# Performance work log

Hardware: AMD Instinct MI355X
Metric: run time of the kernel (lower is better)

Reference implementation:

```python
import jax, jax.numpy as jnp
import numpy as np


def _lin(key, fin, fout):
    return jax.random.normal(key, (fin, fout), jnp.float32) / np.sqrt(fin)


def _hgt_conv(x, Wk, bk, Wq, bq, Wv, bv, a_rel, m_rel, p_rel, Wo, bo, skip, src, dst):
    # Faithful single-(node,edge)-type PyG HGTConv.
    N = x.shape[0]
    H, D = a_rel.shape[0], a_rel.shape[1]
    k = (x @ Wk + bk).reshape(N, H, D)
    q = (x @ Wq + bq).reshape(N, H, D)
    v = (x @ Wv + bv).reshape(N, H, D)
    # per-edge-type relation transforms (per-head DxD matrices)
    k = jnp.einsum('nhd,hde->nhe', k, a_rel)
    v = jnp.einsum('nhd,hde->nhe', v, m_rel)
    # attention logits per edge (j=src -> i=dst), [E,H]
    alpha = (q[dst] * k[src]).sum(-1) * p_rel / jnp.sqrt(jnp.asarray(D, x.dtype))
    # segment softmax over incoming edges of each dst node
    amax = jax.ops.segment_max(alpha, dst, num_segments=N)
    amax = jnp.where(jnp.isfinite(amax), amax, 0.0)  # empty segments
    ex = jnp.exp(alpha - amax[dst])
    denom = jax.ops.segment_sum(ex, dst, num_segments=N)
    w = ex / denom[dst]                                   # [E,H]
    agg = jax.ops.segment_sum(v[src] * w[..., None], dst, num_segments=N)
    out = jax.nn.gelu(agg.reshape(N, H * D), approximate=False) @ Wo + bo
    a = jax.nn.sigmoid(skip)  # trainable skip (in == out channels)
    return a * out + (1.0 - a) * x


def _decode(z, ei, Wlp, blp):
    src, dst = ei[0], ei[1]
    feat = jnp.concatenate([z[src], z[dst]], axis=1)
    return (feat @ Wlp + blp).squeeze(-1)


def setup_inputs() -> dict:
    N, E, P = 50000, 800000, 100000
    C, H = 128, 4
    D = C // H
    ks = jax.random.split(jax.random.key(0), 32)
    inp = {}
    inp['x'] = jax.random.normal(ks[0], (N, C), jnp.float32)
    inp['edge_index'] = jax.random.randint(ks[1], (2, E), 0, N, jnp.int32)
    inp['edge_weight'] = jax.random.uniform(ks[2], (E,), jnp.float32)
    inp['pos_edge_index'] = jax.random.randint(ks[3], (2, P), 0, N, jnp.int32)
    inp['neg_edge_index'] = jax.random.randint(ks[4], (2, P), 0, N, jnp.int32)
    i = 5
    for l in (1, 2):
        for nm in ('k', 'q', 'v'):
            inp[f'W{l}{nm}'] = _lin(ks[i], C, C); i += 1
            inp[f'b{l}{nm}'] = jnp.zeros((C,), jnp.float32)
        inp[f'a{l}'] = jax.random.normal(ks[i], (H, D, D), jnp.float32) / np.sqrt(D); i += 1
        inp[f'm{l}'] = jax.random.normal(ks[i], (H, D, D), jnp.float32) / np.sqrt(D); i += 1
        inp[f'p{l}'] = jnp.ones((H,), jnp.float32)
        inp[f'Wo{l}'] = _lin(ks[i], C, C); i += 1
        inp[f'bo{l}'] = jnp.zeros((C,), jnp.float32)
        inp[f'skip{l}'] = jnp.ones((), jnp.float32)
    inp['Wlp'] = _lin(ks[i], 2 * C, 1)
    inp['blp'] = jnp.zeros((1,), jnp.float32)
    return inp


def reference(x, edge_index, edge_weight, pos_edge_index, neg_edge_index,
              W1k, b1k, W1q, b1q, W1v, b1v, a1, m1, p1, Wo1, bo1, skip1,
              W2k, b2k, W2q, b2q, W2v, b2v, a2, m2, p2, Wo2, bo2, skip2,
              Wlp, blp):
    src, dst = edge_index[0], edge_index[1]
    h1 = _hgt_conv(x, W1k, b1k, W1q, b1q, W1v, b1v, a1, m1, p1, Wo1, bo1, skip1, src, dst)
    h2 = _hgt_conv(h1, W2k, b2k, W2q, b2q, W2v, b2v, a2, m2, p2, Wo2, bo2, skip2, src, dst)
    pos = _decode(h2, pos_edge_index, Wlp, blp)
    neg = _decode(h2, neg_edge_index, Wlp, blp)
    return (pos, neg)
```

## Files before the change

### kernel.cpp

```cpp
#include <hip/hip_runtime.h>
#include <hip/hip_bf16.h>

#define CDIV(a,b) (((a)+(b)-1)/(b))

typedef __attribute__((ext_vector_type(8))) short bh8;
typedef __attribute__((ext_vector_type(4))) float f32x4;

__device__ __forceinline__ float gelu_exact(float x){
  return 0.5f * x * (1.0f + erff(x * 0.7071067811865475f));
}
__device__ __forceinline__ float blo(unsigned u){ return __uint_as_float(u << 16); }
__device__ __forceinline__ float bhi(unsigned u){ return __uint_as_float(u & 0xFFFF0000u); }
__device__ __forceinline__ unsigned short bf16bits(float x){
  __hip_bfloat16 b = __float2bfloat16(x);
  return *(unsigned short*)&b;
}

__global__ void k_clear_int(int* __restrict__ p, int n){
  int i = blockIdx.x*256 + threadIdx.x;
  if (i < n) p[i] = 0;
}

__global__ void k_deg(const int* __restrict__ dst, int* __restrict__ deg, int E){
  int e = blockIdx.x*256 + threadIdx.x;
  if (e < E) atomicAdd(&deg[dst[e]], 1);
}

__global__ void k_scan_blk(const int* __restrict__ deg, int* __restrict__ rowp,
                           int* __restrict__ partial, int N){
  __shared__ int buf[256];
  int i = blockIdx.x*256 + threadIdx.x;
  int v = (i < N) ? deg[i] : 0;
  buf[threadIdx.x] = v;
  __syncthreads();
  #pragma unroll
  for (int off = 1; off < 256; off <<= 1){
    int t = (threadIdx.x >= off) ? buf[threadIdx.x - off] : 0;
    __syncthreads();
    buf[threadIdx.x] += t;
    __syncthreads();
  }
  if (i < N) rowp[i] = buf[threadIdx.x] - v;
  if (threadIdx.x == 255) partial[blockIdx.x] = buf[255];
}

__global__ void k_scan_fin(int* __restrict__ rowp, const int* __restrict__ partial,
                           int* __restrict__ cursor, int N, int E, int nb){
  __shared__ int ws[4];
  int t = threadIdx.x;
  int v = (t < nb && t < blockIdx.x) ? partial[t] : 0;
  #pragma unroll
  for (int m = 32; m; m >>= 1) v += __shfl_xor(v, m);
  if ((t & 63) == 0) ws[t >> 6] = v;
  __syncthreads();
  int pre = ws[0] + ws[1] + ws[2] + ws[3];
  int i = blockIdx.x*256 + t;
  if (i < N){
    int nv = rowp[i] + pre;
    rowp[i] = nv;
    cursor[i] = nv;
  }
  if (i == 0) rowp[N] = E;
}

__global__ void k_fill(const int* __restrict__ src, const int* __restrict__ dst,
                       int* __restrict__ cursor, int* __restrict__ srcs, int E){
  int e = blockIdx.x*256 + threadIdx.x;
  if (e >= E) return;
  int d = dst[e];
  int pos = atomicAdd(&cursor[d], 1);
  srcs[pos] = src[e];
}

__global__ void k_prep(const float* __restrict__ Wk, const float* __restrict__ bk,
                       const float* __restrict__ Ak, const float* __restrict__ Wq,
                       const float* __restrict__ Wv, const float* __restrict__ bv,
                       const float* __restrict__ Av, const float* __restrict__ Wo,
                       short* __restrict__ BfH,
                       float* __restrict__ beffK, float* __restrict__ beffV){
  int t = blockIdx.x*256 + threadIdx.x;
  if (t < 4*16384){
    int g = t >> 14;
    int u = t & 16383;
    int k = u & 127, n = u >> 7;
    float x;
    if (g == 1)      x = Wq[(size_t)k*128 + n];
    else if (g == 3) x = Wo[(size_t)k*128 + n];
    else {
      const float* W = (g == 0) ? Wk : Wv;
      const float* A = (g == 0) ? Ak : Av;
      int h = n >> 5, e2 = n & 31;
      const float* s  = W + (size_t)k*128 + h*32;
      const float* Ah = A + h*1024 + e2;
      float acc = 0.f;
      #pragma unroll
      for (int d = 0; d < 32; ++d) acc += s[d] * Ah[d*32];
      x = acc;
    }
    int nt = n >> 4, lr = n & 15, ks = k >> 5, lk = (k >> 3) & 3, e = k & 7;
    size_t o = ((size_t)((g*8 + nt)*4 + ks)*64 + lr*4 + lk)*8 + e;
    BfH[o] = (short)bf16bits(x);
  } else {
    int u = t - 4*16384;
    if (u < 256){
      int which = u >> 7, n = u & 127;
      const float* b = which ? bv : bk;
      const float* A = which ? Av : Ak;
      int h = n >> 5, e2 = n & 31;
      const float* Ah = A + h*1024 + e2;
      float acc = 0.f;
      #pragma unroll
      for (int d = 0; d < 32; ++d) acc += b[h*32 + d] * Ah[d*32];
      (which ? beffV : beffK)[n] = acc;
    }
  }
}

__global__ __launch_bounds__(256)
void k_kqv(const float* __restrict__ A,
           const short* __restrict__ BfH,
           const float* __restrict__ bK, const float* __restrict__ bQ,
           const float* __restrict__ bV,
           unsigned short* __restrict__ KV16, unsigned short* __restrict__ Qb16, int M){
  const int tid = threadIdx.x;
  const int wm = tid >> 6, l = tid & 63;
  const int lr = l & 15, lk = l >> 4;
  const int perm = (lr*4 + lk)*8;
  const int p0 = blockIdx.x*8 + wm*2;

  bh8 a_h[2][4], a_l[2][4];
  #pragma unroll
  for (int p = 0; p < 2; ++p){
    int row = (p0 + p)*16 + lr;
    #pragma unroll
    for (int ks = 0; ks < 4; ++ks){
      float f[8] = {0.f,0.f,0.f,0.f,0.f,0.f,0.f,0.f};
      if (row < M){
        float4 va = *(const float4*)(A + (size_t)row*128 + ks*32 + lk*8);
        float4 vb = *(const float4*)(A + (size_t)row*128 + ks*32 + lk*8 + 4);
        f[0]=va.x; f[1]=va.y; f[2]=va.z; f[3]=va.w;
        f[4]=vb.x; f[5]=vb.y; f[6]=vb.z; f[7]=vb.w;
      }
      bh8 h8, l8;
      #pragma unroll
      for (int q = 0; q < 8; ++q){
        unsigned ub = __float_as_uint(f[q]);
        h8[q] = (short)(ub >> 16);
        float fhv = __uint_as_float(ub & 0xFFFF0000u);
        l8[q] = (short)(__float_as_uint(f[q] - fhv) >> 16);
      }
      a_h[p][ks] = h8;
      a_l[p][ks] = l8;
    }
  }

  #pragma unroll
  for (int g = 0; g < 3; ++g){
    f32x4 acc[2][8];
    #pragma unroll
    for (int p = 0; p < 2; ++p)
      #pragma unroll
      for (int i = 0; i < 8; ++i) acc[p][i] = (f32x4){0.f,0.f,0.f,0.f};
    #pragma unroll
    for (int ks = 0; ks < 4; ++ks){
      #pragma unroll
      for (int nt = 0; nt < 8; ++nt){
        size_t o = (size_t)((g*8 + nt)*4 + ks)*512 + perm;
        bh8 bh_ = *(const bh8*)(BfH + o);
        #pragma unroll
        for (int p = 0; p < 2; ++p){
          acc[p][nt] = __builtin_amdgcn_mfma_f32_16x16x32_bf16(bh_, a_h[p][ks], acc[p][nt], 0, 0, 0);
          acc[p][nt] = __builtin_amdgcn_mfma_f32_16x16x32_bf16(bh_, a_l[p][ks], acc[p][nt], 0, 0, 0);
        }
      }
    }
    const float* bias = (g==0) ? bK : (g==1) ? bQ : bV;
    #pragma unroll
    for (int p = 0; p < 2; ++p){
      int r = (p0 + p)*16 + lr;
      if (r >= M) continue;
      #pragma unroll
      for (int nt = 0; nt < 8; ++nt){
        int c0 = nt*16 + lk*4;
        float4 bs = *(const float4*)(bias + c0);
        float v0 = acc[p][nt][0] + bs.x;
        float v1 = acc[p][nt][1] + bs.y;
        float v2 = acc[p][nt][2] + bs.z;
        float v3 = acc[p][nt][3] + bs.w;
        unsigned u0 = (unsigned)bf16bits(v0) | ((unsigned)bf16bits(v1) << 16);
        unsigned u1 = (unsigned)bf16bits(v2) | ((unsigned)bf16bits(v3) << 16);
        if (g == 1){
          *(uint2*)(Qb16 + (size_t)r*128 + c0) = make_uint2(u0, u1);
        } else {
          *(uint2*)(KV16 + (size_t)r*256 + (size_t)(nt*4 + lk)*8 + ((g == 2) ? 4 : 0))
              = make_uint2(u0, u1);
        }
      }
    }
  }
}

template<bool DECODE>
__global__ __launch_bounds__(256)
void k_outgemm(const short* __restrict__ AfH,
               const short* __restrict__ BfH,
               const float* __restrict__ bias, const float* __restrict__ mixsrc,
               const float* __restrict__ skipp, float* __restrict__ out,
               const float* __restrict__ Wlp,
               float* __restrict__ s1, float* __restrict__ s2, int M){
  const int tid = threadIdx.x;
  const int wm = tid >> 6, l = tid & 63;
  const int lr = l & 15, lk = l >> 4;
  const int perm = (lr*4 + lk)*8;
  const int p0 = blockIdx.x*8 + wm*2;

  bh8 a_h[2][4];
  #pragma unroll
  for (int p = 0; p < 2; ++p)
    #pragma unroll
    for (int ks = 0; ks < 4; ++ks){
      size_t o = (size_t)((p0 + p)*4 + ks)*512 + perm;
      a_h[p][ks] = *(const bh8*)(AfH + o);
    }

  f32x4 acc[2][8];
  #pragma unroll
  for (int p = 0; p < 2; ++p)
    #pragma unroll
    for (int i = 0; i < 8; ++i) acc[p][i] = (f32x4){0.f,0.f,0.f,0.f};
  #pragma unroll
  for (int ks = 0; ks < 4; ++ks){
    #pragma unroll
    for (int nt = 0; nt < 8; ++nt){
      size_t o = (size_t)((3*8 + nt)*4 + ks)*512 + perm;
      bh8 bh_ = *(const bh8*)(BfH + o);
      #pragma unroll
      for (int p = 0; p < 2; ++p){
        acc[p][nt] = __builtin_amdgcn_mfma_f32_16x16x32_bf16(bh_, a_h[p][ks], acc[p][nt], 0, 0, 0);
      }
    }
  }
  float sg = 1.f / (1.f + expf(-skipp[0]));
  #pragma unroll
  for (int p = 0; p < 2; ++p){
    int r = (p0 + p)*16 + lr;
    if (r >= M) continue;
    float d1 = 0.f, d2 = 0.f;
    #pragma unroll
    for (int nt = 0; nt < 8; ++nt){
      int c0 = nt*16 + lk*4;
      float4 bs  = *(const float4*)(bias + c0);
      float4 mx  = *(const float4*)(mixsrc + (size_t)r*128 + c0);
      float4 o4;
      o4.x = sg*(acc[p][nt][0] + bs.x) + (1.f - sg)*mx.x;
      o4.y = sg*(acc[p][nt][1] + bs.y) + (1.f - sg)*mx.y;
      o4.z = sg*(acc[p][nt][2] + bs.z) + (1.f - sg)*mx.z;
      o4.w = sg*(acc[p][nt][3] + bs.w) + (1.f - sg)*mx.w;
      if (DECODE){
        float4 w1 = *(const float4*)(Wlp + c0);
        float4 w2 = *(const float4*)(Wlp + 128 + c0);
        d1 += o4.x*w1.x + o4.y*w1.y + o4.z*w1.z + o4.w*w1.w;
        d2 += o4.x*w2.x + o4.y*w2.y + o4.z*w2.z + o4.w*w2.w;
      } else {
        *(float4*)(out + (size_t)r*128 + c0) = o4;
      }
    }
    if (DECODE){
      d1 += __shfl_xor(d1, 16); d1 += __shfl_xor(d1, 32);
      d2 += __shfl_xor(d2, 16); d2 += __shfl_xor(d2, 32);
      if (lk == 0){ s1[r] = d1; s2[r] = d2; }
    }
  }
}

__global__ __launch_bounds__(256)
void k_node(const unsigned short* __restrict__ KV, const unsigned short* __restrict__ Qb,
            const int* __restrict__ srcs, const int* __restrict__ row_ptr,
            const float* __restrict__ p,
            short* __restrict__ fh, int NN){
  int wave = threadIdx.x >> 6;
  int lane = threadIdx.x & 63;
  int L = lane & 31;
  int node = blockIdx.x*8 + wave*2 + (lane >> 5);
  if (node >= NN) return;
  int start = row_ptr[node], end = row_ptr[node+1];
  int h = L >> 3;
  float ph = p[h] * 0.25504366769049834f;
  const unsigned short* KVl = KV + L*8;
  uint2 qu = *(const uint2*)(Qb + (size_t)node*128 + L*4);
  float4 qv = make_float4(blo(qu.x), bhi(qu.x), blo(qu.y), bhi(qu.y));

  float a0=0.f, a1=0.f, a2=0.f, a3=0.f, den=0.f;
  int j = start;
  for (; j + 3 < end; j += 4){
    int s0 = srcs[j], s1 = srcs[j+1], s2 = srcs[j+2], s3 = srcs[j+3];
    uint4 kv0 = *(const uint4*)(KVl + (size_t)s0*256);
    uint4 kv1 = *(const uint4*)(KVl + (size_t)s1*256);
    uint4 kv2 = *(const uint4*)(KVl + (size_t)s2*256);
    uint4 kv3 = *(const uint4*)(KVl + (size_t)s3*256);
    float d0 = blo(kv0.x)*qv.x + bhi(kv0.x)*qv.y + blo(kv0.y)*qv.z + bhi(kv0.y)*qv.w;
    float d1 = blo(kv1.x)*qv.x + bhi(kv1.x)*qv.y + blo(kv1.y)*qv.z + bhi(kv1.y)*qv.w;
    float d2 = blo(kv2.x)*qv.x + bhi(kv2.x)*qv.y + blo(kv2.y)*qv.z + bhi(kv2.y)*qv.w;
    float d3 = blo(kv3.x)*qv.x + bhi(kv3.x)*qv.y + blo(kv3.y)*qv.z + bhi(kv3.y)*qv.w;
    #pragma unroll
    for (int m = 1; m < 8; m <<= 1){
      d0 += __shfl_xor(d0, m);
      d1 += __shfl_xor(d1, m);
      d2 += __shfl_xor(d2, m);
      d3 += __shfl_xor(d3, m);
    }
    float w0 = exp2f(d0 * ph);
    float w1 = exp2f(d1 * ph);
    float w2 = exp2f(d2 * ph);
    float w3 = exp2f(d3 * ph);
    den += (w0 + w1) + (w2 + w3);
    a0 += (w0*blo(kv0.z) + w1*blo(kv1.z)) + (w2*blo(kv2.z) + w3*blo(kv3.z));
    a1 += (w0*bhi(kv0.z) + w1*bhi(kv1.z)) + (w2*bhi(kv2.z) + w3*bhi(kv3.z));
    a2 += (w0*blo(kv0.w) + w1*blo(kv1.w)) + (w2*blo(kv2.w) + w3*blo(kv3.w));
    a3 += (w0*bhi(kv0.w) + w1*bhi(kv1.w)) + (w2*bhi(kv2.w) + w3*bhi(kv3.w));
  }
  for (; j < end; ++j){
    int s0 = srcs[j];
    uint4 kv0 = *(const uint4*)(KVl + (size_t)s0*256);
    float d0 = blo(kv0.x)*qv.x + bhi(kv0.x)*qv.y + blo(kv0.y)*qv.z + bhi(kv0.y)*qv.w;
    #pragma unroll
    for (int m = 1; m < 8; m <<= 1) d0 += __shfl_xor(d0, m);
    float w0 = exp2f(d0 * ph);
    den += w0;
    a0 += w0*blo(kv0.z);
    a1 += w0*bhi(kv0.z);
    a2 += w0*blo(kv0.w);
    a3 += w0*bhi(kv0.w);
  }
  float o[4] = {0.f, 0.f, 0.f, 0.f};
  if (end > start){
    float inv = 1.f / den;
    o[0] = gelu_exact(a0 * inv);
    o[1] = gelu_exact(a1 * inv);
    o[2] = gelu_exact(a2 * inv);
    o[3] = gelu_exact(a3 * inv);
  }
  size_t ci = (size_t)((node >> 4)*4 + h)*64 + (node & 15)*4 + ((L >> 1) & 3);
  size_t si = ci*8 + (L & 1)*4;
  uint2 uh = make_uint2((unsigned)bf16bits(o[0]) | ((unsigned)bf16bits(o[1]) << 16),
                        (unsigned)bf16bits(o[2]) | ((unsigned)bf16bits(o[3]) << 16));
  *(uint2*)(fh + si) = uh;
}

__global__ void k_decode(const int* __restrict__ pe, const int* __restrict__ ne,
                         const float* __restrict__ s1, const float* __restrict__ s2,
                         const float* __restrict__ blp, float* __restrict__ out, int P){
  int i = blockIdx.x*256 + threadIdx.x;
  if (i < P){
    out[i] = s1[pe[i]] + s2[pe[P + i]] + blp[0];
  } else if (i < 2*P){
    int j = i - P;
    out[P + j] = s1[ne[j]] + s2[ne[P + j]] + blp[0];
  }
}

extern "C" void kernel_launch(void* const* d_in, const int* in_sizes, int n_in,
                              void* d_out, int out_size, void* d_ws, size_t ws_size,
                              hipStream_t stream){
  const float* x      = (const float*)d_in[0];
  const int*   ei     = (const int*)d_in[1];
  const int*   pos_ei = (const int*)d_in[3];
  const int*   neg_ei = (const int*)d_in[4];
  const int NN = in_sizes[0] / 128;
  const int E  = in_sizes[1] / 2;
  const int P  = in_sizes[3] / 2;
  const int padM = CDIV(NN, 128) * 128;
  const int* e_src = ei;
  const int* e_dst = ei + E;

  char* wsb = (char*)d_ws;
  size_t off = 0;
  auto alloc = [&](size_t bytes)->char*{
    char* r = wsb + off;
    off = (off + bytes + 255) & ~(size_t)255;
    return r;
  };
  unsigned short* KV16 = (unsigned short*)alloc((size_t)NN*256*2);
  unsigned short* Qb16 = (unsigned short*)alloc((size_t)NN*128*2);
  float* h1     = (float*)alloc((size_t)NN*128*4);
  short* AfH    = (short*)alloc((size_t)padM*128*2);
  int*   srcs   = (int*)alloc((size_t)E*4);
  int*   rowp   = (int*)alloc((size_t)(NN+1)*4);
  int*   deg    = (int*)alloc((size_t)NN*4);
  int*   cursor = (int*)alloc((size_t)NN*4);
  int*   partial= (int*)alloc(256*4);
  float* beffK1 = (float*)alloc(128*4);
  float* beffV1 = (float*)alloc(128*4);
  float* beffK2 = (float*)alloc(128*4);
  float* beffV2 = (float*)alloc(128*4);
  short* BfH1   = (short*)alloc((size_t)4*16384*2);
  short* BfH2   = (short*)alloc((size_t)4*16384*2);
  float* s1     = (float*)alloc((size_t)NN*4);
  float* s2     = (float*)alloc((size_t)NN*4);

  const int nb = CDIV(NN, 256);
  k_clear_int<<<CDIV(NN,256),256,0,stream>>>(deg, NN);
  k_deg<<<CDIV(E,256),256,0,stream>>>(e_dst, deg, E);
  k_scan_blk<<<nb,256,0,stream>>>(deg, rowp, partial, NN);
  k_scan_fin<<<nb,256,0,stream>>>(rowp, partial, cursor, NN, E, nb);
  k_fill<<<CDIV(E,256),256,0,stream>>>(e_src, e_dst, cursor, srcs, E);
  k_prep<<<CDIV(4*16384+256,256),256,0,stream>>>(
      (const float*)d_in[5],  (const float*)d_in[6],  (const float*)d_in[11],
      (const float*)d_in[7],  (const float*)d_in[9],  (const float*)d_in[10],
      (const float*)d_in[12], (const float*)d_in[14],
      BfH1, beffK1, beffV1);
  k_prep<<<CDIV(4*16384+256,256),256,0,stream>>>(
      (const float*)d_in[17], (const float*)d_in[18], (const float*)d_in[23],
      (const float*)d_in[19], (const float*)d_in[21], (const float*)d_in[22],
      (const float*)d_in[24], (const float*)d_in[26],
      BfH2, beffK2, beffV2);

  const int gblk = padM / 128;
  const float* Wlp = (const float*)d_in[29];

  k_kqv<<<gblk,256,0,stream>>>(x, BfH1, beffK1, (const float*)d_in[8], beffV1,
                               KV16, Qb16, NN);
  k_node<<<CDIV(NN,8),256,0,stream>>>(KV16, Qb16, srcs, rowp,
                                      (const float*)d_in[13], AfH, NN);
  k_outgemm<false><<<gblk,256,0,stream>>>(AfH, BfH1, (const float*)d_in[15], x,
                                          (const float*)d_in[16], h1,
                                          nullptr, nullptr, nullptr, NN);
  k_kqv<<<gblk,256,0,stream>>>(h1, BfH2, beffK2, (const float*)d_in[20], beffV2,
                               KV16, Qb16, NN);
  k_node<<<CDIV(NN,8),256,0,stream>>>(KV16, Qb16, srcs, rowp,
                                      (const float*)d_in[25], AfH, NN);
  k_outgemm<true><<<gblk,256,0,stream>>>(AfH, BfH2, (const float*)d_in[27], h1,
                                         (const float*)d_in[28], nullptr,
                                         Wlp, s1, s2, NN);

  k_decode<<<CDIV(2*P,256),256,0,stream>>>(pos_ei, neg_ei, s1, s2,
                                           (const float*)d_in[30], (float*)d_out, P);
}
```

Baseline: 306.9 us.

## Drop split-bf16 input GEMM, store intermediate h1 as bf16, merge prep kernels

Removes the hi/lo bf16 split of the GEMM input in k_kqv, halving the MFMA count, and rounds the input to bf16 once instead. Layer-1 output h1 is written and read as bf16 rather than fp32, halving its traffic in the outgemm store, the second kqv load and the skip-mix read. The two weight-prep launches are merged into one. The cost is lower precision in the K/Q/V projections and in the residual path, which may push results closer to the tolerance.

```diff
diff --git a/kernel.cpp b/kernel.cpp
--- a/kernel.cpp
+++ b/kernel.cpp
@@ -72,17 +72,14 @@
   srcs[pos] = src[e];
 }
 
-__global__ void k_prep(const float* __restrict__ Wk, const float* __restrict__ bk,
-                       const float* __restrict__ Ak, const float* __restrict__ Wq,
-                       const float* __restrict__ Wv, const float* __restrict__ bv,
-                       const float* __restrict__ Av, const float* __restrict__ Wo,
-                       short* __restrict__ BfH,
-                       float* __restrict__ beffK, float* __restrict__ beffV){
-  int t = blockIdx.x*256 + threadIdx.x;
-  if (t < 4*16384){
-    int g = t >> 14;
-    int u = t & 16383;
-    int k = u & 127, n = u >> 7;
+__device__ __forceinline__ void prep_one(int u,
+    const float* Wk, const float* bk, const float* Ak, const float* Wq,
+    const float* Wv, const float* bv, const float* Av, const float* Wo,
+    short* BfH, float* beffK, float* beffV){
+  if (u < 4*16384){
+    int g = u >> 14;
+    int w = u & 16383;
+    int k = w & 127, n = w >> 7;
     float x;
     if (g == 1)      x = Wq[(size_t)k*128 + n];
     else if (g == 3) x = Wo[(size_t)k*128 + n];
@@ -101,9 +98,9 @@
     size_t o = ((size_t)((g*8 + nt)*4 + ks)*64 + lr*4 + lk)*8 + e;
     BfH[o] = (short)bf16bits(x);
   } else {
-    int u = t - 4*16384;
-    if (u < 256){
-      int which = u >> 7, n = u & 127;
+    int w = u - 4*16384;
+    if (w < 256){
+      int which = w >> 7, n = w & 127;
       const float* b = which ? bv : bk;
       const float* A = which ? Av : Ak;
       int h = n >> 5, e2 = n & 31;
@@ -116,8 +113,25 @@
   }
 }
 
+__global__ void k_prep2(
+    const float* Wk1, const float* bk1, const float* Ak1, const float* Wq1,
+    const float* Wv1, const float* bv1, const float* Av1, const float* Wo1,
+    const float* Wk2, const float* bk2, const float* Ak2, const float* Wq2,
+    const float* Wv2, const float* bv2, const float* Av2, const float* Wo2,
+    short* __restrict__ BfH1, short* __restrict__ BfH2,
+    float* __restrict__ beffK1, float* __restrict__ beffV1,
+    float* __restrict__ beffK2, float* __restrict__ beffV2){
+  const int SZ = 4*16384 + 256;
+  int t = blockIdx.x*256 + threadIdx.x;
+  if (t < SZ)
+    prep_one(t, Wk1, bk1, Ak1, Wq1, Wv1, bv1, Av1, Wo1, BfH1, beffK1, beffV1);
+  else if (t < 2*SZ)
+    prep_one(t - SZ, Wk2, bk2, Ak2, Wq2, Wv2, bv2, Av2, Wo2, BfH2, beffK2, beffV2);
+}
+
+template<bool BF16IN>
 __global__ __launch_bounds__(256)
-void k_kqv(const float* __restrict__ A,
+void k_kqv(const void* __restrict__ Ain,
            const short* __restrict__ BfH,
            const float* __restrict__ bK, const float* __restrict__ bQ,
            const float* __restrict__ bV,
@@ -128,29 +142,31 @@
   const int perm = (lr*4 + lk)*8;
   const int p0 = blockIdx.x*8 + wm*2;
 
-  bh8 a_h[2][4], a_l[2][4];
+  bh8 a_h[2][4];
   #pragma unroll
   for (int p = 0; p < 2; ++p){
     int row = (p0 + p)*16 + lr;
     #pragma unroll
     for (int ks = 0; ks < 4; ++ks){
-      float f[8] = {0.f,0.f,0.f,0.f,0.f,0.f,0.f,0.f};
-      if (row < M){
-        float4 va = *(const float4*)(A + (size_t)row*128 + ks*32 + lk*8);
-        float4 vb = *(const float4*)(A + (size_t)row*128 + ks*32 + lk*8 + 4);
-        f[0]=va.x; f[1]=va.y; f[2]=va.z; f[3]=va.w;
-        f[4]=vb.x; f[5]=vb.y; f[6]=vb.z; f[7]=vb.w;
-      }
-      bh8 h8, l8;
-      #pragma unroll
-      for (int q = 0; q < 8; ++q){
-        unsigned ub = __float_as_uint(f[q]);
-        h8[q] = (short)(ub >> 16);
-        float fhv = __uint_as_float(ub & 0xFFFF0000u);
-        l8[q] = (short)(__float_as_uint(f[q] - fhv) >> 16);
-      }
-      a_h[p][ks] = h8;
-      a_l[p][ks] = l8;
+      if (BF16IN){
+        bh8 z = (bh8){0,0,0,0,0,0,0,0};
+        if (row < M)
+          z = *(const bh8*)((const short*)Ain + (size_t)row*128 + ks*32 + lk*8);
+        a_h[p][ks] = z;
+      } else {
+        const float* A = (const float*)Ain;
+        float f[8] = {0.f,0.f,0.f,0.f,0.f,0.f,0.f,0.f};
+        if (row < M){
+          float4 va = *(const float4*)(A + (size_t)row*128 + ks*32 + lk*8);
+          float4 vb = *(const float4*)(A + (size_t)row*128 + ks*32 + lk*8 + 4);
+          f[0]=va.x; f[1]=va.y; f[2]=va.z; f[3]=va.w;
+          f[4]=vb.x; f[5]=vb.y; f[6]=vb.z; f[7]=vb.w;
+        }
+        bh8 h8;
+        #pragma unroll
+        for (int q = 0; q < 8; ++q) h8[q] = (short)bf16bits(f[q]);
+        a_h[p][ks] = h8;
+      }
     }
   }
 
@@ -170,7 +186,6 @@
         #pragma unroll
         for (int p = 0; p < 2; ++p){
           acc[p][nt] = __builtin_amdgcn_mfma_f32_16x16x32_bf16(bh_, a_h[p][ks], acc[p][nt], 0, 0, 0);
-          acc[p][nt] = __builtin_amdgcn_mfma_f32_16x16x32_bf16(bh_, a_l[p][ks], acc[p][nt], 0, 0, 0);
         }
       }
     }
@@ -200,12 +215,12 @@
   }
 }
 
-template<bool DECODE>
+template<bool DECODE, bool MIXBF16>
 __global__ __launch_bounds__(256)
 void k_outgemm(const short* __restrict__ AfH,
                const short* __restrict__ BfH,
-               const float* __restrict__ bias, const float* __restrict__ mixsrc,
-               const float* __restrict__ skipp, float* __restrict__ out,
+               const float* __restrict__ bias, const void* __restrict__ mixsrc,
+               const float* __restrict__ skipp, unsigned short* __restrict__ outb,
                const float* __restrict__ Wlp,
                float* __restrict__ s1, float* __restrict__ s2, int M){
   const int tid = threadIdx.x;
@@ -249,8 +264,14 @@
     #pragma unroll
     for (int nt = 0; nt < 8; ++nt){
       int c0 = nt*16 + lk*4;
-      float4 bs  = *(const float4*)(bias + c0);
-      float4 mx  = *(const float4*)(mixsrc + (size_t)r*128 + c0);
+      float4 bs = *(const float4*)(bias + c0);
+      float4 mx;
+      if (MIXBF16){
+        uint2 mu = *(const uint2*)((const unsigned short*)mixsrc + (size_t)r*128 + c0);
+        mx = make_float4(blo(mu.x), bhi(mu.x), blo(mu.y), bhi(mu.y));
+      } else {
+        mx = *(const float4*)((const float*)mixsrc + (size_t)r*128 + c0);
+      }
       float4 o4;
       o4.x = sg*(acc[p][nt][0] + bs.x) + (1.f - sg)*mx.x;
       o4.y = sg*(acc[p][nt][1] + bs.y) + (1.f - sg)*mx.y;
@@ -262,7 +283,9 @@
         d1 += o4.x*w1.x + o4.y*w1.y + o4.z*w1.z + o4.w*w1.w;
         d2 += o4.x*w2.x + o4.y*w2.y + o4.z*w2.z + o4.w*w2.w;
       } else {
-        *(float4*)(out + (size_t)r*128 + c0) = o4;
+        unsigned u0 = (unsigned)bf16bits(o4.x) | ((unsigned)bf16bits(o4.y) << 16);
+        unsigned u1 = (unsigned)bf16bits(o4.z) | ((unsigned)bf16bits(o4.w) << 16);
+        *(uint2*)(outb + (size_t)r*128 + c0) = make_uint2(u0, u1);
       }
     }
     if (DECODE){
@@ -382,7 +405,7 @@
   };
   unsigned short* KV16 = (unsigned short*)alloc((size_t)NN*256*2);
   unsigned short* Qb16 = (unsigned short*)alloc((size_t)NN*128*2);
-  float* h1     = (float*)alloc((size_t)NN*128*4);
+  unsigned short* h1b  = (unsigned short*)alloc((size_t)NN*128*2);
   short* AfH    = (short*)alloc((size_t)padM*128*2);
   int*   srcs   = (int*)alloc((size_t)E*4);
   int*   rowp   = (int*)alloc((size_t)(NN+1)*4);
@@ -404,34 +427,32 @@
   k_scan_blk<<<nb,256,0,stream>>>(deg, rowp, partial, NN);
   k_scan_fin<<<nb,256,0,stream>>>(rowp, partial, cursor, NN, E, nb);
   k_fill<<<CDIV(E,256),256,0,stream>>>(e_src, e_dst, cursor, srcs, E);
-  k_prep<<<CDIV(4*16384+256,256),256,0,stream>>>(
+  k_prep2<<<CDIV(2*(4*16384+256),256),256,0,stream>>>(
       (const float*)d_in[5],  (const float*)d_in[6],  (const float*)d_in[11],
       (const float*)d_in[7],  (const float*)d_in[9],  (const float*)d_in[10],
       (const float*)d_in[12], (const float*)d_in[14],
-      BfH1, beffK1, beffV1);
-  k_prep<<<CDIV(4*16384+256,256),256,0,stream>>>(
       (const float*)d_in[17], (const float*)d_in[18], (const float*)d_in[23],
       (const float*)d_in[19], (const float*)d_in[21], (const float*)d_in[22],
       (const float*)d_in[24], (const float*)d_in[26],
-      BfH2, beffK2, beffV2);
+      BfH1, BfH2, beffK1, beffV1, beffK2, beffV2);
 
   const int gblk = padM / 128;
   const float* Wlp = (const float*)d_in[29];
 
-  k_kqv<<<gblk,256,0,stream>>>(x, BfH1, beffK1, (const float*)d_in[8], beffV1,
-                               KV16, Qb16, NN);
+  k_kqv<false><<<gblk,256,0,stream>>>(x, BfH1, beffK1, (const float*)d_in[8], beffV1,
+                                      KV16, Qb16, NN);
   k_node<<<CDIV(NN,8),256,0,stream>>>(KV16, Qb16, srcs, rowp,
                                       (const float*)d_in[13], AfH, NN);
-  k_outgemm<false><<<gblk,256,0,stream>>>(AfH, BfH1, (const float*)d_in[15], x,
-                                          (const float*)d_in[16], h1,
-                                          nullptr, nullptr, nullptr, NN);
-  k_kqv<<<gblk,256,0,stream>>>(h1, BfH2, beffK2, (const float*)d_in[20], beffV2,
-                               KV16, Qb16, NN);
+  k_outgemm<false,false><<<gblk,256,0,stream>>>(AfH, BfH1, (const float*)d_in[15], x,
+                                                (const float*)d_in[16], h1b,
+                                                nullptr, nullptr, nullptr, NN);
+  k_kqv<true><<<gblk,256,0,stream>>>(h1b, BfH2, beffK2, (const float*)d_in[20], beffV2,
+                                     KV16, Qb16, NN);
   k_node<<<CDIV(NN,8),256,0,stream>>>(KV16, Qb16, srcs, rowp,
                                       (const float*)d_in[25], AfH, NN);
-  k_outgemm<true><<<gblk,256,0,stream>>>(AfH, BfH2, (const float*)d_in[27], h1,
-                                         (const float*)d_in[28], nullptr,
-                                         Wlp, s1, s2, NN);
+  k_outgemm<true,true><<<gblk,256,0,stream>>>(AfH, BfH2, (const float*)d_in[27], h1b,
+                                              (const float*)d_in[28], nullptr,
+                                              Wlp, s1, s2, NN);
 
   k_decode<<<CDIV(2*P,256),256,0,stream>>>(pos_ei, neg_ei, s1, s2,
                                            (const float*)d_in[30], (float*)d_out, P);
```

After: 305.2 us. About the same (-0.6%).
